# Optimization experiments

Measured on AMD Instinct MI355X. Metric: run time of the kernel, lower is better.

The kernel has to match this reference:

```python
import jax, jax.numpy as jnp
import numpy as np

BN_EPS = 1e-5

def conv1x1(t, w, b):
    # t: [B,Cin,H,W], w: [Cout,Cin], b: [Cout]
    return jnp.einsum('bchw,oc->bohw', t, w) + b[None, :, None, None]

def setup_inputs() -> dict:
    key = jax.random.key(0)
    ks = jax.random.split(key, 11)
    B, Cx, Hx, Wx = 8, 64, 128, 64
    Cy, Hy, Wy = 256, 64, 32
    d = Cy // 8  # num_heads=8
    return {
        'x': jax.random.normal(ks[0], (B, Cx, Hx, Wx), jnp.float32),
        'y': jax.random.normal(ks[1], (B, Cy, Hy, Wy), jnp.float32),
        'wq': jax.random.normal(ks[2], (d, Cy), jnp.float32) * 0.05,
        'bq': jax.random.normal(ks[3], (d,), jnp.float32) * 0.05,
        'wk': jax.random.normal(ks[4], (d, Cy), jnp.float32) * 0.05,
        'bk': jax.random.normal(ks[5], (d,), jnp.float32) * 0.05,
        'wv': jax.random.normal(ks[6], (Cx, Cx), jnp.float32) * 0.05,
        'bv': jax.random.normal(ks[7], (Cx,), jnp.float32) * 0.05,
        'gamma': jax.random.normal(ks[8], (1,), jnp.float32),
        'bn_w': jax.random.normal(ks[9], (Cx,), jnp.float32),
        'bn_b': jax.random.normal(ks[10], (Cx,), jnp.float32),
    }

def reference(x, y, wq, bq, wk, bk, wv, bv, gamma, bn_w, bn_b):
    B, Cx, Hx, Wx = x.shape
    _, Cy, Hy, Wy = y.shape
    size_x = Hx * Wx
    size_y = Hy * Wy
    r = size_x // size_y  # nearest-upsample replication factor (integer here)

    q = conv1x1(y, wq, bq).reshape(B, -1, size_y)  # [B,d,Sy]
    k = conv1x1(y, wk, bk).reshape(B, -1, size_y)  # [B,d,Sy]
    energy = jnp.einsum('bds,bdt->bst', q, k)      # [B,Sy,Sy]
    A = jax.nn.softmax(energy, axis=-1)            # [B,Sy,Sy]

    v = conv1x1(x, wv, bv).reshape(B, Cx, size_x)  # [B,Cx,Sx]
    # Nearest upsample of A to [Sx,Sx] with A_up[i,j]=A[i//r, j//r], then
    # out[c,i] = sum_j v[c,j]*A_up[i,j]  ==  repeat( v_pooled @ A^T , r )
    v_pool = v.reshape(B, Cx, size_y, r).sum(-1)   # block-sum over j within each low-res bin
    O = jnp.einsum('bcj,bij->bci', v_pool, A)      # [B,Cx,Sy]
    out = jnp.repeat(O, r, axis=-1)                # replicate along i: index i -> i//r
    out = out.reshape(B, Cx, Hx, Wx)

    out = gamma[0] * out
    # BatchNorm2d (training-mode batch statistics, biased variance)
    mean = out.mean(axis=(0, 2, 3), keepdims=True)
    var = out.var(axis=(0, 2, 3), keepdims=True)
    out = (out - mean) * jax.lax.rsqrt(var + BN_EPS)
    out = out * bn_w[None, :, None, None] + bn_b[None, :, None, None]
    return x + out
```

## Files before the change

kernel.cpp:

```cpp
#include <hip/hip_runtime.h>
#include <hip/hip_bf16.h>

typedef __attribute__((ext_vector_type(8))) short short8;
typedef __attribute__((ext_vector_type(4))) float f32x4;
typedef unsigned short ushort_t;
typedef unsigned int uint_t;

static constexpr int B  = 8;
static constexpr int CX = 64;
static constexpr int SX = 8192;
static constexpr int CY = 256;
static constexpr int SY = 2048;
static constexpr int D  = 32;

static constexpr size_t OFF_Q  = 0;
static constexpr size_t OFF_K  = OFF_Q + (size_t)B*SY*D*2;
static constexpr size_t OFF_V  = OFF_K + (size_t)B*SY*D*2;
static constexpr size_t OFF_O  = OFF_V + (size_t)B*CX*SY*2;
static constexpr size_t OFF_P1 = OFF_O + (size_t)B*CX*SY*4;
static constexpr size_t OFF_P2 = OFF_P1 + 256*64*4;
static constexpr size_t OFF_SC = OFF_P2 + 256*64*4;
static constexpr size_t OFF_SH = OFF_SC + 64*4;

__device__ inline ushort_t f2bf(float f) {
    uint_t u = __builtin_bit_cast(uint_t, f);
    u += 0x7fffu + ((u >> 16) & 1u);
    return (ushort_t)(u >> 16);
}
__device__ inline uint_t pack_bf16(float a, float b) {
    uint_t ua = __builtin_bit_cast(uint_t, a);
    uint_t ub = __builtin_bit_cast(uint_t, b);
    ua += 0x7fffu + ((ua >> 16) & 1u);
    ub += 0x7fffu + ((ub >> 16) & 1u);
    return (ua >> 16) | (ub & 0xffff0000u);
}

__global__ __launch_bounds__(1024) void k_qk(
    const float* __restrict__ y, const float* __restrict__ wq,
    const float* __restrict__ bq, const float* __restrict__ wk,
    const float* __restrict__ bk, ushort_t* __restrict__ qT, ushort_t* __restrict__ kT)
{
    __shared__ __align__(16) float ylds[256][68];
    __shared__ __align__(16) float wlds[256][68];
    const int t  = threadIdx.x;
    const int b  = blockIdx.x >> 5;
    const int s0 = (blockIdx.x & 31) << 6;

    {
        const int c  = t & 255;
        const int rb = (t >> 8) << 4;
#pragma unroll
        for (int i = 0; i < 16; ++i) {
            const int r = rb + i;
            wlds[c][r] = (r < 32) ? wq[r * CY + c] : wk[(r - 32) * CY + c];
        }
    }
    {
        const float4* y4 = reinterpret_cast<const float4*>(y);
#pragma unroll
        for (int p = 0; p < 4; ++p) {
            const int flat = p * 1024 + t;
            const int cc = flat >> 4, s4 = flat & 15;
            const float4 v = y4[(size_t)(b * CY + cc) * (SY / 4) + (s0 >> 2) + s4];
            *reinterpret_cast<float4*>(&ylds[cc][s4 * 4]) = v;
        }
    }
    __syncthreads();

    const int w = t >> 6, s = t & 63;
    float a0 = 0.f, a1 = 0.f, a2 = 0.f, a3 = 0.f;
#pragma unroll 4
    for (int c = 0; c < 256; ++c) {
        const float yv = ylds[c][s];
        const float4 wv = *reinterpret_cast<const float4*>(&wlds[c][w * 4]);
        a0 += wv.x * yv; a1 += wv.y * yv; a2 += wv.z * yv; a3 += wv.w * yv;
    }
    const int o = w * 4;
    float b0, b1, b2, b3;
    if (o < 32) { b0 = bq[o]; b1 = bq[o+1]; b2 = bq[o+2]; b3 = bq[o+3]; }
    else        { b0 = bk[o-32]; b1 = bk[o-31]; b2 = bk[o-30]; b3 = bk[o-29]; }

    __syncthreads();
    ushort_t* qlds = reinterpret_cast<ushort_t*>(&ylds[0][0]);
    {
        uint_t* q32 = reinterpret_cast<uint_t*>(qlds);
        const int base = s * 36 + (o >> 1);
        q32[base]     = pack_bf16(a0 + b0, a1 + b1);
        q32[base + 1] = pack_bf16(a2 + b2, a3 + b3);
    }
    __syncthreads();

    if (t < 512) {
        const int half = t >> 8;
        const int tt = t & 255;
        const int ss = tt >> 2, ch = tt & 3;
        const float4 vv = *reinterpret_cast<const float4*>(&qlds[ss * 72 + half * 32 + ch * 8]);
        ushort_t* dst = half == 0 ? qT : kT;
        reinterpret_cast<float4*>(dst)[(size_t)(b * SY + s0 + ss) * 4 + ch] = vv;
    }
}

__global__ __launch_bounds__(1024) void k_v(
    const float* __restrict__ x, const float* __restrict__ wv,
    const float* __restrict__ bv, ushort_t* __restrict__ vB)
{
    __shared__ __align__(16) float xp[64][68];
    __shared__ __align__(16) float wt[64][68];
    const int t   = threadIdx.x;
    const int b   = blockIdx.x >> 5;
    const int jj0 = (blockIdx.x & 31) << 6;

#pragma unroll
    for (int p = 0; p < 4; ++p) {
        const int f = p * 1024 + t;
        const int co = f >> 6, ci = f & 63;
        wt[ci][co] = wv[co * 64 + ci];
    }
    {
        const float4* x4 = reinterpret_cast<const float4*>(x);
#pragma unroll
        for (int p = 0; p < 4; ++p) {
            const int f = p * 1024 + t;
            const int ci = f >> 6, j = f & 63;
            const float4 v = x4[(size_t)(b * CX + ci) * (SX / 4) + jj0 + j];
            xp[ci][j] = (v.x + v.y) + (v.z + v.w);
        }
    }
    __syncthreads();

    const int w = t >> 6, j = t & 63;
    float a0 = 0.f, a1 = 0.f, a2 = 0.f, a3 = 0.f;
#pragma unroll 4
    for (int ci = 0; ci < 64; ++ci) {
        const float xv = xp[ci][j];
        const float4 w4 = *reinterpret_cast<const float4*>(&wt[ci][w * 4]);
        a0 += w4.x * xv; a1 += w4.y * xv; a2 += w4.z * xv; a3 += w4.w * xv;
    }
    const int c0 = w * 4;
    const size_t base = (size_t)(b * CX) * SY + jj0 + j;
    vB[base + (size_t)(c0 + 0) * SY] = f2bf(a0 + 4.f * bv[c0 + 0]);
    vB[base + (size_t)(c0 + 1) * SY] = f2bf(a1 + 4.f * bv[c0 + 1]);
    vB[base + (size_t)(c0 + 2) * SY] = f2bf(a2 + 4.f * bv[c0 + 2]);
    vB[base + (size_t)(c0 + 3) * SY] = f2bf(a3 + 4.f * bv[c0 + 3]);
}

__global__ __launch_bounds__(1024) void k_attn(
    const ushort_t* __restrict__ qT, const ushort_t* __restrict__ kT,
    const ushort_t* __restrict__ vB, float* __restrict__ O,
    float* __restrict__ part1, float* __restrict__ part2)
{
    __shared__ __align__(16) unsigned char smem[65536];
    unsigned char* Kb0 = smem;
    unsigned char* Kb1 = smem + 8192;
    unsigned char* Vb0 = smem + 16384;
    unsigned char* Vb1 = smem + 32768;
    unsigned char* Pl  = smem + 49152;
    float* Otile = reinterpret_cast<float*>(smem);
    float* Lpart = reinterpret_cast<float*>(smem + 17408);
    float* invL  = reinterpret_cast<float*>(smem + 19456);

    const int t  = threadIdx.x;
    const int w  = t >> 6, l = t & 63;
    const int g  = l >> 4, li = l & 15;
    const int b  = blockIdx.x >> 5;
    const int i0 = (blockIdx.x & 31) << 6;

    const int jtt = w >> 1, h = w & 1;
    const int n   = w & 3,  ks = w >> 2;
    const int m0  = 2 * h, m1 = 2 * h + 1;

    const ushort_t* kb = kT + (size_t)b * SY * D;
    const ushort_t* vb = vB + (size_t)b * CX * SY;

    const short8 qf0 = *reinterpret_cast<const short8*>(
        qT + ((size_t)(b * SY + i0 + m0 * 16 + li)) * D + g * 8);
    const short8 qf1 = *reinterpret_cast<const short8*>(
        qT + ((size_t)(b * SY + i0 + m1 * 16 + li)) * D + g * 8);

    const int koff = w * 1024 + l * 16;
    const int vc = w * 4 + g;
    const int vldso = vc * 256 + li * 16;
    const unsigned char* kgb = reinterpret_cast<const unsigned char*>(kb);
    const unsigned char* vgb = reinterpret_cast<const unsigned char*>(vb)
                             + (size_t)vc * (SY * 2) + ((li ^ (vc & 7)) * 16);

    f32x4 acc[4];
#pragma unroll
    for (int m = 0; m < 4; ++m) acc[m] = (f32x4){0.f, 0.f, 0.f, 0.f};
    float lsum0 = 0.f, lsum1 = 0.f;

    const int swzP = (li & 7) << 4;

    {
        short8 kr, vr;
        if (w < 8) kr = *reinterpret_cast<const short8*>(kgb + koff);
        vr = *reinterpret_cast<const short8*>(vgb);
        if (w < 8) *reinterpret_cast<short8*>(Kb0 + koff) = kr;
        *reinterpret_cast<short8*>(Vb0 + vldso) = vr;
    }
    __syncthreads();

    for (int ch = 0; ch < 16; ++ch) {
        unsigned char* Kc = (ch & 1) ? Kb1 : Kb0;
        unsigned char* Vc = (ch & 1) ? Vb1 : Vb0;
        unsigned char* Kn = (ch & 1) ? Kb0 : Kb1;
        unsigned char* Vn = (ch & 1) ? Vb0 : Vb1;

        short8 kr, vr;
        if (ch < 15) {
            if (w < 8) kr = *reinterpret_cast<const short8*>(kgb + (size_t)(ch + 1) * 8192 + koff);
            vr = *reinterpret_cast<const short8*>(vgb + (size_t)(ch + 1) * 256);
        }

        const short8 kf = *reinterpret_cast<const short8*>(Kc + (jtt * 16 + li) * 64 + g * 16);
        const f32x4 d0 = __builtin_amdgcn_mfma_f32_16x16x32_bf16(kf, qf0, (f32x4){0.f,0.f,0.f,0.f}, 0, 0, 0);
        const f32x4 d1 = __builtin_amdgcn_mfma_f32_16x16x32_bf16(kf, qf1, (f32x4){0.f,0.f,0.f,0.f}, 0, 0, 0);

        {
            const float e0 = __expf(d0[0]), e1 = __expf(d0[1]);
            const float e2 = __expf(d0[2]), e3 = __expf(d0[3]);
            lsum0 += (e0 + e1) + (e2 + e3);
            uint2 pw; pw.x = pack_bf16(e0, e1); pw.y = pack_bf16(e2, e3);
            *reinterpret_cast<uint2*>(Pl + (m0 * 16 + li) * 256 + ((jtt * 32 + g * 8) ^ swzP)) = pw;
        }
        {
            const float e0 = __expf(d1[0]), e1 = __expf(d1[1]);
            const float e2 = __expf(d1[2]), e3 = __expf(d1[3]);
            lsum1 += (e0 + e1) + (e2 + e3);
            uint2 pw; pw.x = pack_bf16(e0, e1); pw.y = pack_bf16(e2, e3);
            *reinterpret_cast<uint2*>(Pl + (m1 * 16 + li) * 256 + ((jtt * 32 + g * 8) ^ swzP)) = pw;
        }
        __syncthreads();

        const short8 vf = *reinterpret_cast<const short8*>(
            Vc + (n * 16 + li) * 256 + ((ks * 64 + g * 16) ^ ((li & 7) << 4)));
#pragma unroll
        for (int m = 0; m < 4; ++m) {
            const short8 pf = *reinterpret_cast<const short8*>(
                Pl + (m * 16 + li) * 256 + ((ks * 64 + g * 16) ^ swzP));
            acc[m] = __builtin_amdgcn_mfma_f32_16x16x32_bf16(pf, vf, acc[m], 0, 0, 0);
        }

        if (ch < 15) {
            if (w < 8) *reinterpret_cast<short8*>(Kn + koff) = kr;
            *reinterpret_cast<short8*>(Vn + vldso) = vr;
        }
        __syncthreads();
    }

    lsum0 += __shfl_xor(lsum0, 16, 64);
    lsum0 += __shfl_xor(lsum0, 32, 64);
    lsum1 += __shfl_xor(lsum1, 16, 64);
    lsum1 += __shfl_xor(lsum1, 32, 64);
    if (l < 16) {
        Lpart[jtt * 64 + m0 * 16 + l] = lsum0;
        Lpart[jtt * 64 + m1 * 16 + l] = lsum1;
    }
    if (ks == 0) {
#pragma unroll
        for (int m = 0; m < 4; ++m) {
            float4 v = make_float4(acc[m][0], acc[m][1], acc[m][2], acc[m][3]);
            *reinterpret_cast<float4*>(&Otile[(n * 16 + li) * 68 + m * 16 + g * 4]) = v;
        }
    }
    __syncthreads();
    if (t < 64) {
        float L = 0.f;
#pragma unroll
        for (int jj = 0; jj < 8; ++jj) L += Lpart[jj * 64 + t];
        invL[t] = 1.f / L;
    }
    if (ks == 1) {
#pragma unroll
        for (int m = 0; m < 4; ++m) {
            float4* p = reinterpret_cast<float4*>(&Otile[(n * 16 + li) * 68 + m * 16 + g * 4]);
            float4 v = *p;
            v.x += acc[m][0]; v.y += acc[m][1]; v.z += acc[m][2]; v.w += acc[m][3];
            *p = v;
        }
    }
    __syncthreads();
    if (ks == 2) {
#pragma unroll
        for (int m = 0; m < 4; ++m) {
            float4* p = reinterpret_cast<float4*>(&Otile[(n * 16 + li) * 68 + m * 16 + g * 4]);
            float4 v = *p;
            v.x += acc[m][0]; v.y += acc[m][1]; v.z += acc[m][2]; v.w += acc[m][3];
            *p = v;
        }
    }
    __syncthreads();
    if (ks == 3) {
#pragma unroll
        for (int m = 0; m < 4; ++m) {
            float4* p = reinterpret_cast<float4*>(&Otile[(n * 16 + li) * 68 + m * 16 + g * 4]);
            float4 v = *p;
            v.x += acc[m][0]; v.y += acc[m][1]; v.z += acc[m][2]; v.w += acc[m][3];
            *p = v;
        }
    }
    __syncthreads();

    if (t < 64) {
        float sa = 0.f, sq = 0.f;
        for (int i = 0; i < 64; ++i) {
            const float v = Otile[t * 68 + i] * invL[i];
            sa += v; sq += v * v;
        }
        part1[blockIdx.x * 64 + t] = sa;
        part2[blockIdx.x * 64 + t] = sq;
    }

    {
        const int c = t >> 4, i4 = t & 15;
        float4 o;
        o.x = Otile[c * 68 + i4 * 4 + 0] * invL[i4 * 4 + 0];
        o.y = Otile[c * 68 + i4 * 4 + 1] * invL[i4 * 4 + 1];
        o.z = Otile[c * 68 + i4 * 4 + 2] * invL[i4 * 4 + 2];
        o.w = Otile[c * 68 + i4 * 4 + 3] * invL[i4 * 4 + 3];
        reinterpret_cast<float4*>(O)[(size_t)(b * CX + c) * (SY / 4) + (i0 >> 2) + i4] = o;
    }
}

__global__ __launch_bounds__(1024) void k_bn(
    const float* __restrict__ part1, const float* __restrict__ part2,
    const float* __restrict__ gamma, const float* __restrict__ bn_w,
    const float* __restrict__ bn_b, float* __restrict__ sc,
    float* __restrict__ sh)
{
    __shared__ float r1[16][64], r2[16][64];
    const int t = threadIdx.x;
    const int c = t & 63, q = t >> 6;
    float s1 = 0.f, s2 = 0.f;
#pragma unroll
    for (int n = 0; n < 16; ++n) {
        const int row = n * 16 + q;
        s1 += part1[row * 64 + c];
        s2 += part2[row * 64 + c];
    }
    r1[q][c] = s1; r2[q][c] = s2;
    __syncthreads();
    if (t < 64) {
        float S1 = 0.f, S2 = 0.f;
#pragma unroll
        for (int k = 0; k < 16; ++k) { S1 += r1[k][t]; S2 += r2[k][t]; }
        const float g = gamma[0];
        const float invN = 1.f / 16384.f;
        const float mean = S1 * invN;
        const float var  = S2 * invN - mean * mean;
        const float inv  = rsqrtf(g * g * var + 1e-5f);
        const float scale = g * inv * bn_w[t];
        sc[t] = scale;
        sh[t] = bn_b[t] - mean * scale;
    }
}

__global__ __launch_bounds__(256) void k_out(
    const float* __restrict__ x, const float* __restrict__ Obuf,
    const float* __restrict__ sc, const float* __restrict__ sh,
    float* __restrict__ out)
{
    const int gid = blockIdx.x * 256 + threadIdx.x;
    const int c = (gid >> 11) & 63;
    const float o  = Obuf[gid];
    const float4 xv = reinterpret_cast<const float4*>(x)[gid];
    const float val = o * sc[c] + sh[c];
    float4 r;
    r.x = xv.x + val; r.y = xv.y + val; r.z = xv.z + val; r.w = xv.w + val;
    reinterpret_cast<float4*>(out)[gid] = r;
}

extern "C" void kernel_launch(void* const* d_in, const int* in_sizes, int n_in,
                              void* d_out, int out_size, void* d_ws, size_t ws_size,
                              hipStream_t stream)
{
    (void)in_sizes; (void)n_in; (void)out_size; (void)ws_size;
    const float* x  = (const float*)d_in[0];
    const float* y  = (const float*)d_in[1];
    const float* wq = (const float*)d_in[2];
    const float* bq = (const float*)d_in[3];
    const float* wk = (const float*)d_in[4];
    const float* bk = (const float*)d_in[5];
    const float* wv = (const float*)d_in[6];
    const float* bv = (const float*)d_in[7];
    const float* gm = (const float*)d_in[8];
    const float* bw = (const float*)d_in[9];
    const float* bb = (const float*)d_in[10];

    char* ws = (char*)d_ws;
    ushort_t* qT  = (ushort_t*)(ws + OFF_Q);
    ushort_t* kT  = (ushort_t*)(ws + OFF_K);
    ushort_t* vBp = (ushort_t*)(ws + OFF_V);
    float*    Ob  = (float*)(ws + OFF_O);
    float*    p1  = (float*)(ws + OFF_P1);
    float*    p2  = (float*)(ws + OFF_P2);
    float*    scp = (float*)(ws + OFF_SC);
    float*    shp = (float*)(ws + OFF_SH);

    k_qk  <<<256, 1024, 0, stream>>>(y, wq, bq, wk, bk, qT, kT);
    k_v   <<<256, 1024, 0, stream>>>(x, wv, bv, vBp);
    k_attn<<<256, 1024, 0, stream>>>(qT, kT, vBp, Ob, p1, p2);
    k_bn  <<<1,   1024, 0, stream>>>(p1, p2, gm, bw, bb, scp, shp);
    k_out <<<4096, 256, 0, stream>>>(x, Ob, scp, shp, (float*)d_out);
}
```

Before: 142.5 us.

## Compute Q/K projection with bf16 MFMA and enlarge partial-stat buffers

Rewrites the Q/K 1x1-conv projection kernel so it converts weights and the y tile to bf16 in swizzled LDS and computes the 64x64 output tile with 16x16x32 bf16 MFMA instructions, replacing the scalar fp32 FMA loop. Results are written directly to qT/kT with bias added, which removes the extra LDS transpose stage and its barriers. The partial-statistics workspace offsets are doubled, likely to fit a change elsewhere, and one V fragment swizzle expression is replaced by a shared variable. Rounding the projection inputs to bf16 lowers the precision of Q and K.

```diff
diff --git a/kernel.cpp b/kernel.cpp
--- a/kernel.cpp
+++ b/kernel.cpp
@@ -18,8 +18,8 @@
 static constexpr size_t OFF_V  = OFF_K + (size_t)B*SY*D*2;
 static constexpr size_t OFF_O  = OFF_V + (size_t)B*CX*SY*2;
 static constexpr size_t OFF_P1 = OFF_O + (size_t)B*CX*SY*4;
-static constexpr size_t OFF_P2 = OFF_P1 + 256*64*4;
-static constexpr size_t OFF_SC = OFF_P2 + 256*64*4;
+static constexpr size_t OFF_P2 = OFF_P1 + 512*64*4;
+static constexpr size_t OFF_SC = OFF_P2 + 512*64*4;
 static constexpr size_t OFF_SH = OFF_SC + 64*4;
 
 __device__ inline ushort_t f2bf(float f) {
@@ -40,64 +40,58 @@
     const float* __restrict__ bq, const float* __restrict__ wk,
     const float* __restrict__ bk, ushort_t* __restrict__ qT, ushort_t* __restrict__ kT)
 {
-    __shared__ __align__(16) float ylds[256][68];
-    __shared__ __align__(16) float wlds[256][68];
+    __shared__ __align__(16) unsigned char Wl[32768];
+    __shared__ __align__(16) unsigned char Yl[32768];
     const int t  = threadIdx.x;
     const int b  = blockIdx.x >> 5;
     const int s0 = (blockIdx.x & 31) << 6;
 
+#pragma unroll
+    for (int p = 0; p < 8; ++p) {
+        const int idx = p * 1024 + t;
+        const int o   = idx >> 7;
+        const int c2  = idx & 127;
+        const float f0 = (o < 32) ? wq[o * CY + 2 * c2]     : wk[(o - 32) * CY + 2 * c2];
+        const float f1 = (o < 32) ? wq[o * CY + 2 * c2 + 1] : wk[(o - 32) * CY + 2 * c2 + 1];
+        *reinterpret_cast<uint_t*>(Wl + ((o * 512 + c2 * 4) ^ ((o & 7) << 4))) = pack_bf16(f0, f1);
+    }
     {
-        const int c  = t & 255;
-        const int rb = (t >> 8) << 4;
-#pragma unroll
-        for (int i = 0; i < 16; ++i) {
-            const int r = rb + i;
-            wlds[c][r] = (r < 32) ? wq[r * CY + c] : wk[(r - 32) * CY + c];
-        }
-    }
-    {
-        const float4* y4 = reinterpret_cast<const float4*>(y);
-#pragma unroll
-        for (int p = 0; p < 4; ++p) {
-            const int flat = p * 1024 + t;
-            const int cc = flat >> 4, s4 = flat & 15;
-            const float4 v = y4[(size_t)(b * CY + cc) * (SY / 4) + (s0 >> 2) + s4];
-            *reinterpret_cast<float4*>(&ylds[cc][s4 * 4]) = v;
-        }
-    }
-    __syncthreads();
-
-    const int w = t >> 6, s = t & 63;
-    float a0 = 0.f, a1 = 0.f, a2 = 0.f, a3 = 0.f;
-#pragma unroll 4
-    for (int c = 0; c < 256; ++c) {
-        const float yv = ylds[c][s];
-        const float4 wv = *reinterpret_cast<const float4*>(&wlds[c][w * 4]);
-        a0 += wv.x * yv; a1 += wv.y * yv; a2 += wv.z * yv; a3 += wv.w * yv;
-    }
-    const int o = w * 4;
-    float b0, b1, b2, b3;
-    if (o < 32) { b0 = bq[o]; b1 = bq[o+1]; b2 = bq[o+2]; b3 = bq[o+3]; }
-    else        { b0 = bk[o-32]; b1 = bk[o-31]; b2 = bk[o-30]; b3 = bk[o-29]; }
-
-    __syncthreads();
-    ushort_t* qlds = reinterpret_cast<ushort_t*>(&ylds[0][0]);
-    {
-        uint_t* q32 = reinterpret_cast<uint_t*>(qlds);
-        const int base = s * 36 + (o >> 1);
-        q32[base]     = pack_bf16(a0 + b0, a1 + b1);
-        q32[base + 1] = pack_bf16(a2 + b2, a3 + b3);
-    }
-    __syncthreads();
-
-    if (t < 512) {
-        const int half = t >> 8;
-        const int tt = t & 255;
-        const int ss = tt >> 2, ch = tt & 3;
-        const float4 vv = *reinterpret_cast<const float4*>(&qlds[ss * 72 + half * 32 + ch * 8]);
-        ushort_t* dst = half == 0 ? qT : kT;
-        reinterpret_cast<float4*>(dst)[(size_t)(b * SY + s0 + ss) * 4 + ch] = vv;
-    }
+        const int l = t & 63, cg = t >> 6;
+        const float* ysrc = y + (size_t)(b * CY + cg * 16) * SY + s0 + l;
+#pragma unroll
+        for (int k = 0; k < 8; ++k) {
+            const float f0 = ysrc[(2 * k)     * SY];
+            const float f1 = ysrc[(2 * k + 1) * SY];
+            const int c = cg * 16 + 2 * k;
+            *reinterpret_cast<uint_t*>(Yl + ((l * 512 + c * 2) ^ ((l & 7) << 4))) = pack_bf16(f0, f1);
+        }
+    }
+    __syncthreads();
+
+    const int w  = t >> 6, l = t & 63;
+    const int li = l & 15, g = l >> 4;
+    const int ot = w & 3,  st = w >> 2;
+    const int oo = ot * 16 + li;
+    const int ss = st * 16 + li;
+
+    f32x4 acc = (f32x4){0.f, 0.f, 0.f, 0.f};
+#pragma unroll
+    for (int ch = 0; ch < 8; ++ch) {
+        const short8 wf = *reinterpret_cast<const short8*>(
+            Wl + ((oo * 512 + ch * 64 + g * 16) ^ ((oo & 7) << 4)));
+        const short8 yf = *reinterpret_cast<const short8*>(
+            Yl + ((ss * 512 + ch * 64 + g * 16) ^ ((ss & 7) << 4)));
+        acc = __builtin_amdgcn_mfma_f32_16x16x32_bf16(wf, yf, acc, 0, 0, 0);
+    }
+    const float* bias = (ot < 2) ? bq : bk;
+    const int ob = (ot & 1) * 16 + g * 4;
+    const float v0 = acc[0] + bias[ob + 0];
+    const float v1 = acc[1] + bias[ob + 1];
+    const float v2 = acc[2] + bias[ob + 2];
+    const float v3 = acc[3] + bias[ob + 3];
+    uint2 pw; pw.x = pack_bf16(v0, v1); pw.y = pack_bf16(v2, v3);
+    ushort_t* dst = (ot < 2) ? qT : kT;
+    *reinterpret_cast<uint2*>(dst + (size_t)(b * SY + s0 + ss) * D + ob) = pw;
 }
 
 __global__ __launch_bounds__(1024) void k_v(
@@ -233,7 +227,7 @@
         __syncthreads();
 
         const short8 vf = *reinterpret_cast<const short8*>(
-            Vc + (n * 16 + li) * 256 + ((ks * 64 + g * 16) ^ ((li & 7) << 4)));
+            Vc + (n * 16 + li) * 256 + ((ks * 64 + g * 16) ^ swzP));
 #pragma unroll
         for (int m = 0; m < 4; ++m) {
             const short8 pf = *reinterpret_cast<const short8*>(
```

After: 133.2 us. -6.6%, faster.
